# Kernel optimization log

Measured on AMD Instinct MI355X. Metric: run time of the kernel, lower is better.

## Reference

```python
import jax, jax.numpy as jnp
import numpy as np

C = 10      # num_clusters; unknown id = C, embedding rows = C+1
I = 512     # input feature dim
D = 256     # gated-attention hidden dim
EMB = 8     # cluster embedding dim
NCLS = 2    # n_classes
B, N = 8, 16384

def setup_inputs() -> dict:
    key = jax.random.key(0)
    ks = jax.random.split(key, 16)
    xn = lambda k, shape, s=0.05: jax.random.normal(k, shape, jnp.float32) * s
    return {
        'h': jax.random.normal(ks[0], (B, N, I), jnp.float32),
        'cluster_ids': jax.random.randint(ks[1], (B, N), 0, C + 1),
        'emb_table': xn(ks[2], (C + 1, EMB), 0.02),
        'W_fuse': xn(ks[3], (I + EMB, I)), 'b_fuse': jnp.zeros((I,), jnp.float32),
        'Wa1': xn(ks[4], (I, D)), 'ba1': jnp.zeros((D,), jnp.float32),
        'Wb1': xn(ks[5], (I, D)), 'bb1': jnp.zeros((D,), jnp.float32),
        'Wc1': xn(ks[6], (D, 1)), 'bc1': jnp.zeros((1,), jnp.float32),
        'W_intra': xn(ks[7], (I, 512)), 'b_intra': jnp.zeros((512,), jnp.float32),
        'Wa2': xn(ks[8], (512, D)), 'ba2': jnp.zeros((D,), jnp.float32),
        'Wb2': xn(ks[9], (512, D)), 'bb2': jnp.zeros((D,), jnp.float32),
        'Wc2': xn(ks[10], (D, 1)), 'bc2': jnp.zeros((1,), jnp.float32),
        'W_inter': xn(ks[11], (512, 256)), 'b_inter': jnp.zeros((256,), jnp.float32),
        'W_cls': xn(ks[12], (256, NCLS)), 'b_cls': jnp.zeros((NCLS,), jnp.float32),
    }

def _forward(h, cluster_ids, emb_table, W_fuse, b_fuse, Wa1, ba1, Wb1, bb1, Wc1, bc1,
             W_intra, b_intra, Wa2, ba2, Wb2, bb2, Wc2, bc2, W_inter, b_inter, W_cls, b_cls):
    Bn, Nn, Idim = h.shape
    cids = jnp.clip(cluster_ids, 0, C)
    # cluster-id embedding fusion: concat + Linear + ReLU
    x = jnp.concatenate([h, emb_table[cids]], axis=-1)          # [B,N,I+EMB]
    x = jax.nn.relu(x @ W_fuse + b_fuse)                        # [B,N,I]
    # intra-cluster gated attention scores
    a = jnp.tanh(x @ Wa1 + ba1)
    g = jax.nn.sigmoid(x @ Wb1 + bb1)
    A = ((a * g) @ Wc1 + bc1)[..., 0]                           # [B,N]
    # segment softmax per (batch, cluster id) -- replaces the per-cluster Python loop
    seg = (jnp.arange(Bn)[:, None] * (C + 1) + cids).reshape(-1)  # [B*N]
    nseg = Bn * (C + 1)
    Af = A.reshape(-1)
    seg_max = jax.ops.segment_max(Af, seg, num_segments=nseg)
    seg_max = jnp.where(jnp.isfinite(seg_max), seg_max, 0.0)
    ex = jnp.exp(Af - seg_max[seg])
    denom = jax.ops.segment_sum(ex, seg, num_segments=nseg)
    w = ex / denom[seg]                                          # [B*N]
    xf = x.reshape(Bn * Nn, Idim)
    cfeat = jax.ops.segment_sum(xf * w[:, None], seg, num_segments=nseg)  # [B*(C+1),I]
    counts = jax.ops.segment_sum(jnp.ones_like(Af), seg, num_segments=nseg)
    present = (counts > 0).reshape(Bn, C + 1)
    cfeat = jax.nn.relu(cfeat @ W_intra + b_intra).reshape(Bn, C + 1, 512)
    # inter-cluster gated attention (empty clusters masked out of softmax)
    a2 = jnp.tanh(cfeat @ Wa2 + ba2)
    g2 = jax.nn.sigmoid(cfeat @ Wb2 + bb2)
    A2 = ((a2 * g2) @ Wc2 + bc2)[..., 0]                         # [B,C+1]
    A2 = jnp.where(present, A2, -jnp.inf)
    Ws = jax.nn.softmax(A2, axis=1)
    slide = jnp.einsum('bc,bcf->bf', Ws, cfeat)                  # [B,512]
    slide = jax.nn.relu(slide @ W_inter + b_inter)               # [B,256]
    return slide @ W_cls + b_cls                                 # [B,n_classes]

def reference(h, cluster_ids, emb_table, W_fuse, b_fuse, Wa1, ba1, Wb1, bb1, Wc1, bc1,
              W_intra, b_intra, Wa2, ba2, Wb2, bb2, Wc2, bc2, W_inter, b_inter, W_cls, b_cls):
    return _forward(h, cluster_ids, emb_table, W_fuse, b_fuse, Wa1, ba1, Wb1, bb1, Wc1, bc1,
                    W_intra, b_intra, Wa2, ba2, Wb2, bb2, Wc2, bc2, W_inter, b_inter, W_cls, b_cls)
```

## Files before the change

kernel.cpp:

```cpp
#include <hip/hip_runtime.h>
#include <stdint.h>

typedef __bf16 bf16;
typedef __bf16 bf16x8 __attribute__((ext_vector_type(8)));
typedef __bf16 bf16x4 __attribute__((ext_vector_type(4)));
typedef __bf16 bf16x2 __attribute__((ext_vector_type(2)));
typedef float  f32x4  __attribute__((ext_vector_type(4)));
typedef float  fvec4  __attribute__((ext_vector_type(4)));

static const size_t OFF_A       = 0;
static const size_t OFF_SEGMAX  = 524288;
static const size_t OFF_DENOM   = 524800;
static const size_t OFF_CNT     = 525312;
static const size_t OFF_CFEAT   = 525824;
static const size_t OFF_CFEAT2  = 706048;
static const size_t ZERO_BYTES  = 886272;
static const size_t OFF_FLAG    = 886272;
static const size_t OFF_CANON   = 886336;
static const size_t OFF_TEMB    = 894528;
static const size_t OFF_X       = 917056;
static const size_t OFF_WFT     = OFF_X + (size_t)134217728;
static const size_t OFF_WGT     = OFF_WFT + 524288;
static const size_t OFF_WINTRAT = OFF_WGT + 524288;
static const size_t OFF_WA2T    = OFF_WINTRAT + 524288;
static const size_t OFF_WB2T    = OFF_WA2T + 262144;
static const size_t OFF_WINTERT = OFF_WB2T + 262144;
static const size_t OFF_A2V     = OFF_WINTERT + 262144;

#define CAN_BA1    0
#define CAN_BB1    256
#define CAN_WC1    512
#define CAN_BINTRA 768
#define CAN_BA2    1280
#define CAN_BB2    1536
#define CAN_WC2    1792
#define CAN_BINTER 2048
#define CAN_WCLS   2304
#define CAN_BCLS   2816

__device__ __forceinline__ int clip11(int c) { return c < 0 ? 0 : (c > 10 ? 10 : c); }

__device__ __forceinline__ float relu_f(float v) { return v < 0.0f ? 0.0f : v; }

__device__ __forceinline__ float fast_tanh(float a) {
  return 1.f - 2.f / (1.f + __expf(2.f * a));
}

__device__ __forceinline__ float cvt(const void* p, int i, int fl) {
  return fl ? ((const float*)p)[i] : (float)((const bf16*)p)[i];
}

__device__ __forceinline__ unsigned fkey(float f) {
  unsigned u = __float_as_uint(f);
  return (u & 0x80000000u) ? ~u : (u | 0x80000000u);
}
__device__ __forceinline__ float key_to_f(unsigned k) {
  unsigned u = (k & 0x80000000u) ? (k & 0x7FFFFFFFu) : ~k;
  return __uint_as_float(u);
}

__device__ __forceinline__ void async16(const void* g, void* l) {
  __builtin_amdgcn_global_load_lds(
      (const __attribute__((address_space(1))) unsigned int*)g,
      (__attribute__((address_space(3))) unsigned int*)l, 16, 0, 0);
}

#define VMCNT(n)  asm volatile("s_waitcnt vmcnt(" #n ")" ::: "memory")
#define LGKMCNT0  asm volatile("s_waitcnt lgkmcnt(0)" ::: "memory")
#define SBAR      __builtin_amdgcn_s_barrier()


__device__ __forceinline__ void stageB512(const bf16* __restrict__ src, bf16* lds,
                                          int lane, int wid) {
#pragma unroll
  for (int j = 0; j < 512; j += 64) {
    const int row = j + wid * 16 + (lane >> 2);
    const int gs  = (lane & 3) ^ ((row >> 1) & 3);
    async16(src + (size_t)row * 512 + gs * 8, lds + (j + wid * 16) * 32);
  }
}

struct AHold { fvec4 v0, v1; bf16x4 b0, b1; };
__device__ __forceinline__ void loadA(AHold& h, const void* __restrict__ src, int fl,
                                      size_t m0, int k0, int tid) {
  const int row = tid >> 2, slot = tid & 3;
  const int gs  = slot ^ ((row >> 1) & 3);
  if (fl) {
    const float* gp = (const float*)src + (m0 + row) * 512 + k0 + gs * 8;
    h.v0 = *(const fvec4*)gp;
    h.v1 = *(const fvec4*)(gp + 4);
  } else {
    const bf16* gp = (const bf16*)src + (m0 + row) * 512 + k0 + gs * 8;
    h.b0 = *(const bf16x4*)gp;
    h.b1 = *(const bf16x4*)(gp + 4);
  }
}
__device__ __forceinline__ void writeA(const AHold& h, bf16* lds, int fl, int tid) {
  const int row = tid >> 2, slot = tid & 3;
  bf16x8 b;
  if (fl) {
    b[0]=(bf16)h.v0[0]; b[1]=(bf16)h.v0[1]; b[2]=(bf16)h.v0[2]; b[3]=(bf16)h.v0[3];
    b[4]=(bf16)h.v1[0]; b[5]=(bf16)h.v1[1]; b[6]=(bf16)h.v1[2]; b[7]=(bf16)h.v1[3];
  } else {
    b[0]=h.b0[0]; b[1]=h.b0[1]; b[2]=h.b0[2]; b[3]=h.b0[3];
    b[4]=h.b1[0]; b[5]=h.b1[1]; b[6]=h.b1[2]; b[7]=h.b1[3];
  }
  *(bf16x8*)(lds + row * 32 + slot * 8) = b;
}

__global__ void k_detect(const unsigned short* __restrict__ hh, int* __restrict__ flag) {
  const int lane = threadIdx.x;
  const unsigned short u = hh[lane * 2];
  const int e = (u >> 7) & 0xFF;
  int pl = (e > 96 && e < 140) ? 1 : 0;
#pragma unroll
  for (int off = 1; off < 64; off <<= 1) pl += __shfl_xor(pl, off, 64);
  if (lane == 0) *flag = (pl < 32) ? 1 : 0;
}

#define GEMM_PIPE(ASRC, FL, BSRC)                                              \
  {                                                                            \
    AHold ah;                                                                  \
    loadA(ah, ASRC, FL, m0, 0, tid);                                           \
    stageB512(BSRC, Bs[0], lane, wid);                                         \
    VMCNT(8);                                                                  \
    writeA(ah, As[0], FL, tid);                                                \
    loadA(ah, ASRC, FL, m0, 32, tid);                                          \
    stageB512(BSRC + 32, Bs[1], lane, wid);                                    \
    VMCNT(10);                                                                 \
    LGKMCNT0;                                                                  \
    SBAR;                                                                      \
    for (int t = 0; t < 16; ++t) {                                             \
      const int c = t & 1;                                                     \
      bf16x8 af[4], bfr[8];                                                    \
      _Pragma("unroll")                                                        \
      for (int tt = 0; tt < 4; ++tt)                                           \
        af[tt] = *(const bf16x8*)&As[c][(tt * 16 + l15) * 32 + so];            \
      _Pragma("unroll")                                                        \
      for (int tt = 0; tt < 8; ++tt)                                           \
        bfr[tt] = *(const bf16x8*)&Bs[c][(wid * 128 + tt * 16 + l15) * 32 + so];\
      _Pragma("unroll")                                                        \
      for (int tm = 0; tm < 4; ++tm)                                           \
        _Pragma("unroll")                                                      \
        for (int tn = 0; tn < 8; ++tn)                                         \
          acc[tm][tn] = __builtin_amdgcn_mfma_f32_16x16x32_bf16(               \
              af[tm], bfr[tn], acc[tm][tn], 0, 0, 0);                          \
      if (t < 15) {                                                            \
        SBAR;            \
        VMCNT(8);                                       \
        writeA(ah, As[c ^ 1], FL, tid);                                        \
        if (t < 14) {                                                          \
          loadA(ah, ASRC, FL, m0, (t + 2) * 32, tid);                          \
          stageB512(BSRC + (t + 2) * 32, Bs[c], lane, wid);                    \
          VMCNT(10);          \
        } else {                                                               \
          VMCNT(0);                                    \
        }                                                                      \
        LGKMCNT0;                                                              \
        SBAR;                                                                  \
      }                                                                        \
    }                                                                          \
  }

__global__ __launch_bounds__(256, 2) void k_fuse(
    const void* __restrict__ h, const int* __restrict__ cids,
    const bf16* __restrict__ WfT, const float* __restrict__ Temb,
    const int* __restrict__ flag, bf16* __restrict__ x) {
  __shared__ __align__(16) bf16 As[2][64 * 32];
  __shared__ __align__(16) bf16 Bs[2][512 * 32];
  const int tid = threadIdx.x, lane = tid & 63, wid = tid >> 6;
  const int quad = lane >> 4, l15 = lane & 15;
  const size_t m0 = (size_t)blockIdx.x * 64;
  const int fl = *flag;
  const int so = ((quad ^ ((l15 >> 1) & 3)) << 3);

  f32x4 acc[4][8] = {};
  GEMM_PIPE(h, fl, WfT);

#pragma unroll
  for (int tm = 0; tm < 4; ++tm) {
#pragma unroll
    for (int r = 0; r < 4; ++r) {
      const size_t m = m0 + tm * 16 + quad * 4 + r;
      const int c = clip11(cids[m]);
      const float* Trow = Temb + c * 512;
#pragma unroll
      for (int tn = 0; tn < 8; ++tn) {
        const int nn = wid * 128 + tn * 16 + l15;
        x[m * 512 + nn] = (bf16)relu_f(acc[tm][tn][r] + Trow[nn]);
      }
    }
  }
}

__global__ __launch_bounds__(256, 2) void k_gate1(
    const bf16* __restrict__ x, const bf16* __restrict__ WgT,
    const bf16* __restrict__ canon, float* __restrict__ Apart) {
  __shared__ __align__(16) bf16 As[2][64 * 32];
  __shared__ __align__(16) bf16 Bs[2][512 * 32];
  __shared__ float tok[64];
  const int tid = threadIdx.x, lane = tid & 63, wid = tid >> 6;
  const int quad = lane >> 4, l15 = lane & 15;
  const size_t m0 = (size_t)blockIdx.x * 64;
  const int so = ((quad ^ ((l15 >> 1) & 3)) << 3);

  f32x4 acc[4][8] = {};
  GEMM_PIPE(x, 0, WgT);

  if (tid < 64) tok[tid] = 0.f;
  __syncthreads();
  float bav[4], bbv[4], wcv[4];
#pragma unroll
  for (int p = 0; p < 4; ++p) {
    const int d = wid * 64 + p * 16 + l15;
    bav[p] = (float)canon[CAN_BA1 + d];
    bbv[p] = (float)canon[CAN_BB1 + d];
    wcv[p] = (float)canon[CAN_WC1 + d];
  }
#pragma unroll
  for (int tm = 0; tm < 4; ++tm) {
#pragma unroll
    for (int r = 0; r < 4; ++r) {
      float rs = 0.f;
#pragma unroll
      for (int p = 0; p < 4; ++p) {
        const float a = acc[tm][2 * p][r] + bav[p];
        const float g = acc[tm][2 * p + 1][r] + bbv[p];
        rs += fast_tanh(a) * (1.f / (1.f + __expf(-g))) * wcv[p];
      }
      rs += __shfl_xor(rs, 1, 64);
      rs += __shfl_xor(rs, 2, 64);
      rs += __shfl_xor(rs, 4, 64);
      rs += __shfl_xor(rs, 8, 64);
      if (l15 == 0) atomicAdd(&tok[tm * 16 + quad * 4 + r], rs);
    }
  }
  __syncthreads();
  if (tid < 64) Apart[m0 + tid] = tok[tid];
}

__global__ __launch_bounds__(256) void k_segmax(
    const float* __restrict__ Apart, const int* __restrict__ cids, unsigned* __restrict__ gmax) {
  __shared__ unsigned sm[88];
  const int tid = threadIdx.x;
  if (tid < 88) sm[tid] = 0u;
  __syncthreads();
  const int base = blockIdx.x * 1024;
  const int b = blockIdx.x >> 4;
#pragma unroll
  for (int it = 0; it < 4; ++it) {
    const int t = base + it * 256 + tid;
    atomicMax(&sm[b * 11 + clip11(cids[t])], fkey(Apart[t]));
  }
  __syncthreads();
  if (tid < 88) atomicMax(&gmax[tid], sm[tid]);
}

__global__ __launch_bounds__(256) void k_segsum(
    const float* __restrict__ Apart, const int* __restrict__ cids,
    const unsigned* __restrict__ gmax, float* __restrict__ denom, int* __restrict__ counts) {
  __shared__ float sd[88];
  __shared__ int sc[88];
  const int tid = threadIdx.x;
  if (tid < 88) { sd[tid] = 0.f; sc[tid] = 0; }
  __syncthreads();
  const int base = blockIdx.x * 1024;
  const int b = blockIdx.x >> 4;
#pragma unroll
  for (int it = 0; it < 4; ++it) {
    const int t = base + it * 256 + tid;
    const int seg = b * 11 + clip11(cids[t]);
    atomicAdd(&sd[seg], __expf(Apart[t] - key_to_f(gmax[seg])));
    atomicAdd(&sc[seg], 1);
  }
  __syncthreads();
  if (tid < 88) {
    atomicAdd(&denom[tid], sd[tid]);
    atomicAdd(&counts[tid], sc[tid]);
  }
}

__global__ __launch_bounds__(256) void k_cfeat(
    const float* __restrict__ Apart, const int* __restrict__ cids,
    const unsigned* __restrict__ gmax, const float* __restrict__ denom,
    const bf16* __restrict__ x, float* __restrict__ cfeat) {
  __shared__ float accf[11 * 512];
  __shared__ float wbuf[512];
  __shared__ unsigned char cbuf[512];
  const int tid = threadIdx.x;
  const int base = blockIdx.x * 512;
  const int b = blockIdx.x >> 5;
  for (int i = tid; i < 11 * 512; i += 256) accf[i] = 0.f;
#pragma unroll
  for (int it = 0; it < 2; ++it) {
    const int t = base + it * 256 + tid;
    const int c = clip11(cids[t]);
    const int seg = b * 11 + c;
    wbuf[it * 256 + tid] = __expf(Apart[t] - key_to_f(gmax[seg])) / denom[seg];
    cbuf[it * 256 + tid] = (unsigned char)c;
  }
  __syncthreads();
  const bf16* xp = x + (size_t)base * 512 + tid * 2;
#pragma unroll 4
  for (int i = 0; i < 512; ++i) {
    const float w = wbuf[i];
    const int c = cbuf[i];
    bf16x2 v = *(const bf16x2*)(xp + (size_t)i * 512);
    accf[c * 512 + tid * 2]     += w * (float)v[0];
    accf[c * 512 + tid * 2 + 1] += w * (float)v[1];
  }
  __syncthreads();
  float* cf = cfeat + (size_t)b * 11 * 512;
  for (int i = tid; i < 11 * 512; i += 256)
    atomicAdd(&cf[i], accf[i]);
}

__device__ __forceinline__ float block_sum(float v, float* red, int tid) {
#pragma unroll
  for (int off = 32; off > 0; off >>= 1) v += __shfl_xor(v, off, 64);
  __syncthreads();
  if ((tid & 63) == 0) red[tid >> 6] = v;
  __syncthreads();
  return red[0] + red[1] + red[2] + red[3];
}

__global__ __launch_bounds__(256) void k_intra(
    const float* __restrict__ cfeat, const bf16* __restrict__ WintraT,
    const bf16* __restrict__ Wa2T, const bf16* __restrict__ Wb2T,
    const bf16* __restrict__ canon, float* __restrict__ cfeat2,
    float* __restrict__ A2v) {
  __shared__ float row[512];
  __shared__ float rowo[512];
  __shared__ float red[4];
  const int r = blockIdx.x, tid = threadIdx.x;
  row[tid] = cfeat[(size_t)r * 512 + tid];
  row[tid + 256] = cfeat[(size_t)r * 512 + 256 + tid];
  __syncthreads();
#pragma unroll
  for (int hh = 0; hh < 2; ++hh) {
    const int n = hh * 256 + tid;
    float acc = (float)canon[CAN_BINTRA + n];
    const bf16* wp = WintraT + (size_t)n * 512;
#pragma unroll 4
    for (int k = 0; k < 512; k += 8) {
      bf16x8 wv = *(const bf16x8*)(wp + k);
#pragma unroll
      for (int j = 0; j < 8; ++j) acc += row[k + j] * (float)wv[j];
    }
    const float v = relu_f(acc);
    cfeat2[(size_t)r * 512 + n] = v;
    rowo[n] = v;
  }
  __syncthreads();
  float da = (float)canon[CAN_BA2 + tid], dg = (float)canon[CAN_BB2 + tid];
  const bf16* wa = Wa2T + (size_t)tid * 512;
  const bf16* wb = Wb2T + (size_t)tid * 512;
#pragma unroll 4
  for (int k = 0; k < 512; k += 8) {
    bf16x8 av = *(const bf16x8*)(wa + k);
    bf16x8 gv = *(const bf16x8*)(wb + k);
#pragma unroll
    for (int j = 0; j < 8; ++j) {
      const float rv = rowo[k + j];
      da += rv * (float)av[j];
      dg += rv * (float)gv[j];
    }
  }
  const float contrib = fast_tanh(da) * (1.f / (1.f + __expf(-dg))) * (float)canon[CAN_WC2 + tid];
  const float tot = block_sum(contrib, red, tid);
  if (tid == 0) A2v[r] = tot;
}

__global__ __launch_bounds__(256) void k_tail(
    const float* __restrict__ cfeat2, const float* __restrict__ A2v,
    const int* __restrict__ counts, const bf16* __restrict__ WinterT,
    const bf16* __restrict__ canon, const int* __restrict__ flag,
    void* __restrict__ out) {
  const int b = blockIdx.x, tid = threadIdx.x;
  __shared__ float Wsm[11];
  __shared__ float red[4];
  __shared__ float slide[512];
  __shared__ float hid[256];
  const float* cf = cfeat2 + (size_t)b * 11 * 512;

  if (tid == 0) {
    float mx = -1e30f;
    for (int c = 0; c < 11; ++c)
      if (counts[b * 11 + c] > 0 && A2v[b * 11 + c] > mx) mx = A2v[b * 11 + c];
    float s = 0.f;
    for (int c = 0; c < 11; ++c) {
      const float e = (counts[b * 11 + c] > 0) ? __expf(A2v[b * 11 + c] - mx) : 0.f;
      Wsm[c] = e; s += e;
    }
    for (int c = 0; c < 11; ++c) Wsm[c] /= s;
  }
  __syncthreads();
  float s0 = 0.f, s1 = 0.f;
#pragma unroll
  for (int c = 0; c < 11; ++c) {
    const float w = Wsm[c];
    s0 += w * cf[c * 512 + tid];
    s1 += w * cf[c * 512 + 256 + tid];
  }
  slide[tid] = s0; slide[tid + 256] = s1;
  __syncthreads();
  {
    float acc = (float)canon[CAN_BINTER + tid];
    const bf16* wp = WinterT + (size_t)tid * 512;
#pragma unroll 4
    for (int k = 0; k < 512; k += 8) {
      bf16x8 wv = *(const bf16x8*)(wp + k);
#pragma unroll
      for (int j = 0; j < 8; ++j) acc += slide[k + j] * (float)wv[j];
    }
    hid[tid] = relu_f(acc);
  }
  __syncthreads();
  const float p0 = hid[tid] * (float)canon[CAN_WCLS + tid * 2 + 0];
  const float p1 = hid[tid] * (float)canon[CAN_WCLS + tid * 2 + 1];
  const float t0 = block_sum(p0, red, tid);
  const float t1 = block_sum(p1, red, tid);
  if (tid == 0) {
    const float o0 = t0 + (float)canon[CAN_BCLS + 0];
    const float o1 = t1 + (float)canon[CAN_BCLS + 1];
    if (*flag) {
      ((float*)out)[b * 2 + 0] = o0;
      ((float*)out)[b * 2 + 1] = o1;
    } else {
      ((bf16*)out)[b * 2 + 0] = (bf16)o0;
      ((bf16*)out)[b * 2 + 1] = (bf16)o1;
    }
  }
}

__global__ __launch_bounds__(256) void k_prep(
    const void* __restrict__ Wf, const void* __restrict__ bfuse, const void* __restrict__ emb,
    const void* __restrict__ Wa1, const void* __restrict__ Wb1, const void* __restrict__ Wintra,
    const void* __restrict__ Wa2, const void* __restrict__ Wb2, const void* __restrict__ Winter,
    const void* __restrict__ ba1, const void* __restrict__ bb1, const void* __restrict__ wc1,
    const void* __restrict__ bintra, const void* __restrict__ ba2, const void* __restrict__ bb2,
    const void* __restrict__ wc2, const void* __restrict__ binter, const void* __restrict__ Wcls,
    const void* __restrict__ bcls, const int* __restrict__ flag,
    bf16* __restrict__ WfT, bf16* __restrict__ WgT,
    bf16* __restrict__ WintraT, bf16* __restrict__ Wa2T, bf16* __restrict__ Wb2T,
    bf16* __restrict__ WinterT, float* __restrict__ Temb, bf16* __restrict__ canon) {
  const int fl = *flag;
  int id = blockIdx.x * 256 + threadIdx.x;
  if (id < 262144) { WfT[id] = (bf16)cvt(Wf, (id & 511) * 512 + (id >> 9), fl); return; }
  id -= 262144;
  if (id < 262144) {
    const int r = id >> 9, k = id & 511;
    const int d = ((r >> 5) << 4) | (r & 15);
    WgT[id] = (bf16)cvt(((r >> 4) & 1) ? Wb1 : Wa1, k * 256 + d, fl);
    return;
  }
  id -= 262144;
  if (id < 262144) { WintraT[id] = (bf16)cvt(Wintra, (id & 511) * 512 + (id >> 9), fl); return; }
  id -= 262144;
  if (id < 131072) { Wa2T[id] = (bf16)cvt(Wa2, (id & 511) * 256 + (id >> 9), fl); return; }
  id -= 131072;
  if (id < 131072) { Wb2T[id] = (bf16)cvt(Wb2, (id & 511) * 256 + (id >> 9), fl); return; }
  id -= 131072;
  if (id < 131072) { WinterT[id] = (bf16)cvt(Winter, (id & 511) * 256 + (id >> 9), fl); return; }
  id -= 131072;
  if (id < 5632) {
    const int c = id >> 9, n = id & 511;
    float s = cvt(bfuse, n, fl);
#pragma unroll
    for (int j = 0; j < 8; ++j) s += cvt(emb, c * 8 + j, fl) * cvt(Wf, (512 + j) * 512 + n, fl);
    Temb[id] = s;
    return;
  }
  id -= 5632;
  if (id < 4096) {
    bf16 v = (bf16)0.0f;
    if (id < 256)        v = (bf16)cvt(ba1, id, fl);
    else if (id < 512)   v = (bf16)cvt(bb1, id - 256, fl);
    else if (id < 768)   v = (bf16)cvt(wc1, id - 512, fl);
    else if (id < 1280)  v = (bf16)cvt(bintra, id - 768, fl);
    else if (id < 1536)  v = (bf16)cvt(ba2, id - 1280, fl);
    else if (id < 1792)  v = (bf16)cvt(bb2, id - 1536, fl);
    else if (id < 2048)  v = (bf16)cvt(wc2, id - 1792, fl);
    else if (id < 2304)  v = (bf16)cvt(binter, id - 2048, fl);
    else if (id < 2816)  v = (bf16)cvt(Wcls, id - 2304, fl);
    else if (id < 2818)  v = (bf16)cvt(bcls, id - 2816, fl);
    canon[id] = v;
  }
}

extern "C" void kernel_launch(void* const* d_in, const int* in_sizes, int n_in,
                              void* d_out, int out_size, void* d_ws, size_t ws_size,
                              hipStream_t stream) {
  (void)in_sizes; (void)n_in; (void)out_size; (void)ws_size;
  const void* h      = d_in[0];
  const int*  cids   = (const int*)d_in[1];
  const void* emb    = d_in[2];
  const void* Wf     = d_in[3];
  const void* bfuse  = d_in[4];
  const void* Wa1    = d_in[5];
  const void* ba1    = d_in[6];
  const void* Wb1    = d_in[7];
  const void* bb1    = d_in[8];
  const void* wc1    = d_in[9];
  const void* Wintra = d_in[11];
  const void* bintra = d_in[12];
  const void* Wa2    = d_in[13];
  const void* ba2    = d_in[14];
  const void* Wb2    = d_in[15];
  const void* bb2    = d_in[16];
  const void* wc2    = d_in[17];
  const void* Winter = d_in[19];
  const void* binter = d_in[20];
  const void* Wcls   = d_in[21];
  const void* bcls   = d_in[22];

  char* ws = (char*)d_ws;
  float*    Apart   = (float*)(ws + OFF_A);
  unsigned* gmax    = (unsigned*)(ws + OFF_SEGMAX);
  float*    denom   = (float*)(ws + OFF_DENOM);
  int*      counts  = (int*)(ws + OFF_CNT);
  float*    cfeat   = (float*)(ws + OFF_CFEAT);
  float*    cfeat2  = (float*)(ws + OFF_CFEAT2);
  int*      flag    = (int*)(ws + OFF_FLAG);
  bf16*     canon   = (bf16*)(ws + OFF_CANON);
  float*    Temb    = (float*)(ws + OFF_TEMB);
  bf16*     x       = (bf16*)(ws + OFF_X);
  bf16*     WfT     = (bf16*)(ws + OFF_WFT);
  bf16*     WgT     = (bf16*)(ws + OFF_WGT);
  bf16*     WintraT = (bf16*)(ws + OFF_WINTRAT);
  bf16*     Wa2T    = (bf16*)(ws + OFF_WA2T);
  bf16*     Wb2T    = (bf16*)(ws + OFF_WB2T);
  bf16*     WinterT = (bf16*)(ws + OFF_WINTERT);
  float*    A2v     = (float*)(ws + OFF_A2V);

  hipMemsetAsync(d_ws, 0, ZERO_BYTES, stream);
  k_detect<<<1, 64, 0, stream>>>((const unsigned short*)h, flag);
  k_prep<<<4646, 256, 0, stream>>>(Wf, bfuse, emb, Wa1, Wb1, Wintra, Wa2, Wb2, Winter,
                                   ba1, bb1, wc1, bintra, ba2, bb2, wc2, binter, Wcls, bcls,
                                   flag, WfT, WgT, WintraT, Wa2T, Wb2T, WinterT, Temb, canon);
  k_fuse<<<2048, 256, 0, stream>>>(h, cids, WfT, Temb, flag, x);
  k_gate1<<<2048, 256, 0, stream>>>(x, WgT, canon, Apart);
  k_segmax<<<128, 256, 0, stream>>>(Apart, cids, gmax);
  k_segsum<<<128, 256, 0, stream>>>(Apart, cids, gmax, denom, counts);
  k_cfeat<<<256, 256, 0, stream>>>(Apart, cids, gmax, denom, x, cfeat);
  k_intra<<<88, 256, 0, stream>>>(cfeat, WintraT, Wa2T, Wb2T, canon, cfeat2, A2v);
  k_tail<<<8, 256, 0, stream>>>(cfeat2, A2v, counts, WinterT, canon, flag, d_out);
}
```

Measured before the change: 720.2 us.

## Deepen GEMM A prefetch, tile weight transposes, vectorize cfeat accumulation

The GEMM pipeline now holds two A register buffers so A loads are issued two k-steps ahead instead of one. The loop is unrolled by two and the vmcnt waits are retuned to match. Weight transposes in k_prep move from per-element strided reads to 64x64 LDS tiled transposes with vector loads and stores, which cuts the block count sharply. k_cfeat switches to 256-token blocks where each thread reads 8 bf16 at once and accumulates with LDS atomics. The deeper prefetch adds register pressure, and the LDS atomics may contend.

```diff
diff --git a/kernel.cpp b/kernel.cpp
--- a/kernel.cpp
+++ b/kernel.cpp
@@ -68,6 +68,7 @@
 #define VMCNT(n)  asm volatile("s_waitcnt vmcnt(" #n ")" ::: "memory")
 #define LGKMCNT0  asm volatile("s_waitcnt lgkmcnt(0)" ::: "memory")
 #define SBAR      __builtin_amdgcn_s_barrier()
+#define FENCE     asm volatile("" ::: "memory")
 
 
 __device__ __forceinline__ void stageB512(const bf16* __restrict__ src, bf16* lds,
@@ -118,47 +119,58 @@
   if (lane == 0) *flag = (pl < 32) ? 1 : 0;
 }
 
+#define GEMM_COMPUTE(BUF)                                                      \
+  {                                                                            \
+    bf16x8 af[4], bfr[8];                                                      \
+    _Pragma("unroll") for (int q = 0; q < 4; ++q)                              \
+      af[q] = *(const bf16x8*)&As[BUF][(q * 16 + l15) * 32 + so];              \
+    _Pragma("unroll") for (int q = 0; q < 8; ++q)                              \
+      bfr[q] = *(const bf16x8*)&Bs[BUF][(wid * 128 + q * 16 + l15) * 32 + so]; \
+    _Pragma("unroll") for (int tm = 0; tm < 4; ++tm)                           \
+      _Pragma("unroll") for (int tn = 0; tn < 8; ++tn)                         \
+        acc[tm][tn] = __builtin_amdgcn_mfma_f32_16x16x32_bf16(                 \
+            af[tm], bfr[tn], acc[tm][tn], 0, 0, 0);                            \
+  }
+
+#define GEMM_ITER(T, AH, ASRC, FL, BSRC)                                       \
+  {                                                                            \
+    GEMM_COMPUTE((T) & 1);                                                     \
+    if ((T) < 15) {                                                            \
+      SBAR;                                                                    \
+      VMCNT(10);                                                               \
+      if ((T) <= 13) writeA(AH, As[(T) & 1], FL, tid);                         \
+      if ((T) <= 11) loadA(AH, ASRC, FL, m0, ((T) + 4) * 32, tid);             \
+      FENCE;                                                                   \
+      if ((T) <= 13) stageB512(BSRC + ((T) + 2) * 32, Bs[(T) & 1], lane, wid); \
+      if ((T) <= 11)      { VMCNT(10); }                                       \
+      else if ((T) <= 13) { VMCNT(8); }                                        \
+      else                { VMCNT(0); }                                        \
+      LGKMCNT0;                                                                \
+      SBAR;                                                                    \
+    }                                                                          \
+  }
+
 #define GEMM_PIPE(ASRC, FL, BSRC)                                              \
   {                                                                            \
-    AHold ah;                                                                  \
-    loadA(ah, ASRC, FL, m0, 0, tid);                                           \
+    AHold hA, hB;                                                              \
+    loadA(hA, ASRC, FL, m0, 0, tid);                                           \
+    loadA(hB, ASRC, FL, m0, 32, tid);                                          \
+    FENCE;                                                                     \
     stageB512(BSRC, Bs[0], lane, wid);                                         \
-    VMCNT(8);                                                                  \
-    writeA(ah, As[0], FL, tid);                                                \
-    loadA(ah, ASRC, FL, m0, 32, tid);                                          \
+    VMCNT(10);                             \
+    writeA(hA, As[0], FL, tid);                                                \
+    loadA(hA, ASRC, FL, m0, 64, tid);                                          \
+    VMCNT(10);                             \
+    writeA(hB, As[1], FL, tid);                                                \
+    loadA(hB, ASRC, FL, m0, 96, tid);                                          \
+    FENCE;                                                                     \
     stageB512(BSRC + 32, Bs[1], lane, wid);                                    \
-    VMCNT(10);                                                                 \
+    VMCNT(12);                        \
     LGKMCNT0;                                                                  \
     SBAR;                                                                      \
-    for (int t = 0; t < 16; ++t) {                                             \
-      const int c = t & 1;                                                     \
-      bf16x8 af[4], bfr[8];                                                    \
-      _Pragma("unroll")                                                        \
-      for (int tt = 0; tt < 4; ++tt)                                           \
-        af[tt] = *(const bf16x8*)&As[c][(tt * 16 + l15) * 32 + so];            \
-      _Pragma("unroll")                                                        \
-      for (int tt = 0; tt < 8; ++tt)                                           \
-        bfr[tt] = *(const bf16x8*)&Bs[c][(wid * 128 + tt * 16 + l15) * 32 + so];\
-      _Pragma("unroll")                                                        \
-      for (int tm = 0; tm < 4; ++tm)                                           \
-        _Pragma("unroll")                                                      \
-        for (int tn = 0; tn < 8; ++tn)                                         \
-          acc[tm][tn] = __builtin_amdgcn_mfma_f32_16x16x32_bf16(               \
-              af[tm], bfr[tn], acc[tm][tn], 0, 0, 0);                          \
-      if (t < 15) {                                                            \
-        SBAR;            \
-        VMCNT(8);                                       \
-        writeA(ah, As[c ^ 1], FL, tid);                                        \
-        if (t < 14) {                                                          \
-          loadA(ah, ASRC, FL, m0, (t + 2) * 32, tid);                          \
-          stageB512(BSRC + (t + 2) * 32, Bs[c], lane, wid);                    \
-          VMCNT(10);          \
-        } else {                                                               \
-          VMCNT(0);                                    \
-        }                                                                      \
-        LGKMCNT0;                                                              \
-        SBAR;                                                                  \
-      }                                                                        \
+    for (int tt = 0; tt < 16; tt += 2) {                                       \
+      GEMM_ITER(tt,     hA, ASRC, FL, BSRC);                                   \
+      GEMM_ITER(tt + 1, hB, ASRC, FL, BSRC);                                   \
     }                                                                          \
   }
 
@@ -285,29 +297,31 @@
     const unsigned* __restrict__ gmax, const float* __restrict__ denom,
     const bf16* __restrict__ x, float* __restrict__ cfeat) {
   __shared__ float accf[11 * 512];
-  __shared__ float wbuf[512];
-  __shared__ unsigned char cbuf[512];
+  __shared__ float wbuf[256];
+  __shared__ unsigned char cbuf[256];
   const int tid = threadIdx.x;
-  const int base = blockIdx.x * 512;
-  const int b = blockIdx.x >> 5;
+  const int base = blockIdx.x * 256;
+  const int b = blockIdx.x >> 6;
   for (int i = tid; i < 11 * 512; i += 256) accf[i] = 0.f;
-#pragma unroll
-  for (int it = 0; it < 2; ++it) {
-    const int t = base + it * 256 + tid;
+  {
+    const int t = base + tid;
     const int c = clip11(cids[t]);
     const int seg = b * 11 + c;
-    wbuf[it * 256 + tid] = __expf(Apart[t] - key_to_f(gmax[seg])) / denom[seg];
-    cbuf[it * 256 + tid] = (unsigned char)c;
-  }
-  __syncthreads();
-  const bf16* xp = x + (size_t)base * 512 + tid * 2;
-#pragma unroll 4
-  for (int i = 0; i < 512; ++i) {
-    const float w = wbuf[i];
-    const int c = cbuf[i];
-    bf16x2 v = *(const bf16x2*)(xp + (size_t)i * 512);
-    accf[c * 512 + tid * 2]     += w * (float)v[0];
-    accf[c * 512 + tid * 2 + 1] += w * (float)v[1];
+    wbuf[tid] = __expf(Apart[t] - key_to_f(gmax[seg])) / denom[seg];
+    cbuf[tid] = (unsigned char)c;
+  }
+  __syncthreads();
+  const int co = (tid & 63) * 8;
+  const int tg = tid >> 6;
+#pragma unroll 2
+  for (int it = 0; it < 64; ++it) {
+    const int tk = it * 4 + tg;
+    const float w = wbuf[tk];
+    const int c = cbuf[tk];
+    bf16x8 v = *(const bf16x8*)(x + (size_t)(base + tk) * 512 + co);
+    float* ap = &accf[c * 512 + co];
+#pragma unroll
+    for (int j = 0; j < 8; ++j) atomicAdd(&ap[j], w * (float)v[j]);
   }
   __syncthreads();
   float* cf = cfeat + (size_t)b * 11 * 512;
@@ -433,6 +447,35 @@
   }
 }
 
+__device__ __forceinline__ void tile_transpose(
+    const void* __restrict__ src, bf16* __restrict__ dst, int C, int fl,
+    int tr, int tc, int tid, float* lds ) {
+  const int r = tid >> 2, c0 = (tid & 3) * 16;
+  float* lp = lds + r * 68 + c0;
+  if (fl) {
+    const float* sp = (const float*)src + (size_t)(tr * 64 + r) * C + tc * 64 + c0;
+    fvec4 a = *(const fvec4*)sp, b = *(const fvec4*)(sp + 4),
+          c2 = *(const fvec4*)(sp + 8), d = *(const fvec4*)(sp + 12);
+    *(fvec4*)lp = a; *(fvec4*)(lp + 4) = b;
+    *(fvec4*)(lp + 8) = c2; *(fvec4*)(lp + 12) = d;
+  } else {
+    const bf16* sp = (const bf16*)src + (size_t)(tr * 64 + r) * C + tc * 64 + c0;
+    bf16x8 a = *(const bf16x8*)sp, b = *(const bf16x8*)(sp + 8);
+#pragma unroll
+    for (int j = 0; j < 8; ++j) { lp[j] = (float)a[j]; lp[8 + j] = (float)b[j]; }
+  }
+  __syncthreads();
+  const int dr = tid >> 2, j0 = (tid & 3) * 16;
+  bf16x8 o0, o1;
+#pragma unroll
+  for (int j = 0; j < 8; ++j) {
+    o0[j] = (bf16)lds[(j0 + j) * 68 + dr];
+    o1[j] = (bf16)lds[(j0 + 8 + j) * 68 + dr];
+  }
+  bf16* dp = dst + (size_t)(tc * 64 + dr) * 512 + tr * 64 + j0;
+  *(bf16x8*)dp = o0; *(bf16x8*)(dp + 8) = o1;
+}
+
 __global__ __launch_bounds__(256) void k_prep(
     const void* __restrict__ Wf, const void* __restrict__ bfuse, const void* __restrict__ emb,
     const void* __restrict__ Wa1, const void* __restrict__ Wb1, const void* __restrict__ Wintra,
@@ -444,25 +487,55 @@
     bf16* __restrict__ WfT, bf16* __restrict__ WgT,
     bf16* __restrict__ WintraT, bf16* __restrict__ Wa2T, bf16* __restrict__ Wb2T,
     bf16* __restrict__ WinterT, float* __restrict__ Temb, bf16* __restrict__ canon) {
+  __shared__ float lds[4608];
   const int fl = *flag;
-  int id = blockIdx.x * 256 + threadIdx.x;
-  if (id < 262144) { WfT[id] = (bf16)cvt(Wf, (id & 511) * 512 + (id >> 9), fl); return; }
-  id -= 262144;
-  if (id < 262144) {
-    const int r = id >> 9, k = id & 511;
-    const int d = ((r >> 5) << 4) | (r & 15);
-    WgT[id] = (bf16)cvt(((r >> 4) & 1) ? Wb1 : Wa1, k * 256 + d, fl);
+  const int blk = blockIdx.x, tid = threadIdx.x;
+  if (blk < 64)  { tile_transpose(Wf,     WfT,     512, fl, blk & 7,  blk >> 3, tid, lds); return; }
+  if (blk < 128) { const int t = blk - 64;
+                   tile_transpose(Wintra, WintraT, 512, fl, t & 7,    t >> 3,   tid, lds); return; }
+  if (blk < 192) {
+    const int t = blk - 128, tb = t >> 3, kt = t & 7;
+    float* LA = lds;
+    float* LB = lds + 2304;
+    const int kr = tid >> 2, d0 = (tid & 3) * 8;
+    if (fl) {
+      const float* pa = (const float*)Wa1 + (size_t)(kt * 64 + kr) * 256 + tb * 32 + d0;
+      const float* pb = (const float*)Wb1 + (size_t)(kt * 64 + kr) * 256 + tb * 32 + d0;
+      fvec4 a0 = *(const fvec4*)pa, a1 = *(const fvec4*)(pa + 4);
+      fvec4 b0 = *(const fvec4*)pb, b1 = *(const fvec4*)(pb + 4);
+      *(fvec4*)(LA + kr * 36 + d0) = a0; *(fvec4*)(LA + kr * 36 + d0 + 4) = a1;
+      *(fvec4*)(LB + kr * 36 + d0) = b0; *(fvec4*)(LB + kr * 36 + d0 + 4) = b1;
+    } else {
+      const bf16* pa = (const bf16*)Wa1 + (size_t)(kt * 64 + kr) * 256 + tb * 32 + d0;
+      const bf16* pb = (const bf16*)Wb1 + (size_t)(kt * 64 + kr) * 256 + tb * 32 + d0;
+      bf16x8 a = *(const bf16x8*)pa, b = *(const bf16x8*)pb;
+#pragma unroll
+      for (int j = 0; j < 8; ++j) {
+        LA[kr * 36 + d0 + j] = (float)a[j];
+        LB[kr * 36 + d0 + j] = (float)b[j];
+      }
+    }
+    __syncthreads();
+    const int rr = tid >> 2, j0 = (tid & 3) * 16;
+    const int dl = (((rr >> 5) & 1) << 4) | (rr & 15);
+    const float* Lsrc = ((rr >> 4) & 1) ? LB : LA;
+    bf16x8 o0, o1;
+#pragma unroll
+    for (int j = 0; j < 8; ++j) {
+      o0[j] = (bf16)Lsrc[(j0 + j) * 36 + dl];
+      o1[j] = (bf16)Lsrc[(j0 + 8 + j) * 36 + dl];
+    }
+    bf16* dp = WgT + (size_t)(tb * 64 + rr) * 512 + kt * 64 + j0;
+    *(bf16x8*)dp = o0; *(bf16x8*)(dp + 8) = o1;
     return;
   }
-  id -= 262144;
-  if (id < 262144) { WintraT[id] = (bf16)cvt(Wintra, (id & 511) * 512 + (id >> 9), fl); return; }
-  id -= 262144;
-  if (id < 131072) { Wa2T[id] = (bf16)cvt(Wa2, (id & 511) * 256 + (id >> 9), fl); return; }
-  id -= 131072;
-  if (id < 131072) { Wb2T[id] = (bf16)cvt(Wb2, (id & 511) * 256 + (id >> 9), fl); return; }
-  id -= 131072;
-  if (id < 131072) { WinterT[id] = (bf16)cvt(Winter, (id & 511) * 256 + (id >> 9), fl); return; }
-  id -= 131072;
+  if (blk < 224) { const int t = blk - 192;
+                   tile_transpose(Wa2,    Wa2T,    256, fl, t & 7, t >> 3, tid, lds); return; }
+  if (blk < 256) { const int t = blk - 224;
+                   tile_transpose(Wb2,    Wb2T,    256, fl, t & 7, t >> 3, tid, lds); return; }
+  if (blk < 288) { const int t = blk - 256;
+                   tile_transpose(Winter, WinterT, 256, fl, t & 7, t >> 3, tid, lds); return; }
+  int id = (blk - 288) * 256 + tid;
   if (id < 5632) {
     const int c = id >> 9, n = id & 511;
     float s = cvt(bfuse, n, fl);
@@ -535,14 +608,14 @@
 
   hipMemsetAsync(d_ws, 0, ZERO_BYTES, stream);
   k_detect<<<1, 64, 0, stream>>>((const unsigned short*)h, flag);
-  k_prep<<<4646, 256, 0, stream>>>(Wf, bfuse, emb, Wa1, Wb1, Wintra, Wa2, Wb2, Winter,
-                                   ba1, bb1, wc1, bintra, ba2, bb2, wc2, binter, Wcls, bcls,
-                                   flag, WfT, WgT, WintraT, Wa2T, Wb2T, WinterT, Temb, canon);
+  k_prep<<<326, 256, 0, stream>>>(Wf, bfuse, emb, Wa1, Wb1, Wintra, Wa2, Wb2, Winter,
+                                  ba1, bb1, wc1, bintra, ba2, bb2, wc2, binter, Wcls, bcls,
+                                  flag, WfT, WgT, WintraT, Wa2T, Wb2T, WinterT, Temb, canon);
   k_fuse<<<2048, 256, 0, stream>>>(h, cids, WfT, Temb, flag, x);
   k_gate1<<<2048, 256, 0, stream>>>(x, WgT, canon, Apart);
   k_segmax<<<128, 256, 0, stream>>>(Apart, cids, gmax);
   k_segsum<<<128, 256, 0, stream>>>(Apart, cids, gmax, denom, counts);
-  k_cfeat<<<256, 256, 0, stream>>>(Apart, cids, gmax, denom, x, cfeat);
+  k_cfeat<<<512, 256, 0, stream>>>(Apart, cids, gmax, denom, x, cfeat);
   k_intra<<<88, 256, 0, stream>>>(cfeat, WintraT, Wa2T, Wb2T, canon, cfeat2, A2v);
   k_tail<<<8, 256, 0, stream>>>(cfeat2, A2v, counts, WinterT, canon, flag, d_out);
 }
```

After: 984.2 us. +36.7%, slower.
